# Optimization experiments

Hardware: AMD Instinct MI355X
Metric: run time of the kernel (lower is better)

Reference implementation:

```python
import jax, jax.numpy as jnp
import numpy as np


def setup_inputs() -> dict:
    key = jax.random.key(0)
    k1, k2 = jax.random.split(key)
    pred = jax.random.normal(k1, (1, 2048, 512), dtype=jnp.float32)
    cand = jax.random.normal(k2, (1, 65536, 512), dtype=jnp.float32)
    return {
        "predicted_transaction_company": pred,
        "future_transaction_companies_inc_current_data": cand,
    }


def reference(predicted_transaction_company, future_transaction_companies_inc_current_data):
    # torch.cdist with p=2 on [1,P,D] x [1,R,D] -> [1,P,R]; squeeze(0) -> [P,R]; global min.
    x = predicted_transaction_company[0]                       # [P, D]
    y = future_transaction_companies_inc_current_data[0]       # [R, D]
    sq = (
        jnp.sum(x * x, axis=-1)[:, None]
        + jnp.sum(y * y, axis=-1)[None, :]
        - 2.0 * jnp.einsum("pd,rd->pr", x, y)
    )                                                          # [P, R]
    distances = jnp.sqrt(jnp.maximum(sq, 0.0))
    return jnp.min(distances)
```

## Files before the change

### kernel.cpp

```cpp
#include <hip/hip_runtime.h>
#include <stdint.h>

#define P 2048
#define R 65536
#define DD 512
#define BT 128
#define BK 64

typedef __attribute__((ext_vector_type(8))) short short8;
typedef __attribute__((ext_vector_type(4))) float f32x4;

__device__ inline unsigned short f2bf(float f) {
  unsigned int u = __float_as_uint(f);
  u += 0x7fffu + ((u >> 16) & 1u);
  return (unsigned short)(u >> 16);
}

__device__ inline void gload_lds16(const void* g, void* l) {
  __builtin_amdgcn_global_load_lds(
      (const __attribute__((address_space(1))) unsigned int*)g,
      (__attribute__((address_space(3))) unsigned int*)l,
      16, 0, 0);
}

__global__ __launch_bounds__(256) void k_convert(
    const float* __restrict__ pred, const float* __restrict__ cand,
    unsigned short* __restrict__ Abf, unsigned short* __restrict__ Bbf,
    float* __restrict__ nx, float* __restrict__ ny,
    unsigned int* __restrict__ minp)
{
  if (blockIdx.x == 0 && threadIdx.x == 0) *minp = 0x7f800000u;
  int gw   = (blockIdx.x * 256 + threadIdx.x) >> 6;
  int lane = threadIdx.x & 63;
  if (gw >= P + R) return;
  const float* src; unsigned short* dst; float* np;
  if (gw < P) { src = pred + (size_t)gw * DD; dst = Abf + (size_t)gw * DD; np = nx + gw; }
  else { int r = gw - P; src = cand + (size_t)r * DD; dst = Bbf + (size_t)r * DD; np = ny + r; }
  const float4* s4 = ((const float4*)src) + lane * 2;
  float4 v0 = s4[0], v1 = s4[1];
  float ss = v0.x*v0.x + v0.y*v0.y + v0.z*v0.z + v0.w*v0.w
           + v1.x*v1.x + v1.y*v1.y + v1.z*v1.z + v1.w*v1.w;
  union { unsigned short h[8]; uint4 v; } pk;
  pk.h[0]=f2bf(v0.x); pk.h[1]=f2bf(v0.y); pk.h[2]=f2bf(v0.z); pk.h[3]=f2bf(v0.w);
  pk.h[4]=f2bf(v1.x); pk.h[5]=f2bf(v1.y); pk.h[6]=f2bf(v1.z); pk.h[7]=f2bf(v1.w);
  *(uint4*)(dst + (size_t)lane * 8) = pk.v;
  #pragma unroll
  for (int off = 32; off; off >>= 1) ss += __shfl_down(ss, off, 64);
  if (lane == 0) *np = ss;
}

__global__ __launch_bounds__(256) void k_gemm_min(
    const unsigned short* __restrict__ Abf, const unsigned short* __restrict__ Bbf,
    const float* __restrict__ nx, const float* __restrict__ ny,
    unsigned int* __restrict__ minp)
{
  __shared__ __align__(16) unsigned short As[BT * BK];
  __shared__ __align__(16) unsigned short Bs[BT * BK];
  __shared__ float wmin[4];

  const int tid  = threadIdx.x;
  const int wave = tid >> 6;
  const int lane = tid & 63;
  const int by = blockIdx.x & 15;
  const int bx = blockIdx.x >> 4;
  const int rowA0 = by * BT, rowB0 = bx * BT;
  const int wr = wave >> 1, wc = wave & 1;

  f32x4 zero = {0.f, 0.f, 0.f, 0.f};
  f32x4 acc[4][4];
  #pragma unroll
  for (int i = 0; i < 4; ++i)
    #pragma unroll
    for (int j = 0; j < 4; ++j) acc[i][j] = zero;

  const int rloc = lane >> 3;
  const int cswz = (lane & 7) ^ rloc;
  const unsigned short* gA[4]; const unsigned short* gB[4];
  unsigned short* lA[4]; unsigned short* lB[4];
  #pragma unroll
  for (int t = 0; t < 4; ++t) {
    const int rr = (wave * 4 + t) * 8 + rloc;
    gA[t] = Abf + (size_t)(rowA0 + rr) * DD + cswz * 8;
    gB[t] = Bbf + (size_t)(rowB0 + rr) * DD + cswz * 8;
    lA[t] = As + (wave * 4 + t) * 512;
    lB[t] = Bs + (wave * 4 + t) * 512;
  }

  const int m = lane & 15, quad = lane >> 4, mb = m & 7;
  const unsigned short* apB = As + (wr * 64 + m) * BK;
  const unsigned short* bpB = Bs + (wc * 64 + m) * BK;
  const int sw0 = ((quad    ) ^ mb) * 8;
  const int sw1 = ((quad + 4) ^ mb) * 8;

  for (int k0 = 0; k0 < DD; k0 += BK) {
    #pragma unroll
    for (int t = 0; t < 4; ++t) {
      gload_lds16(gA[t] + k0, lA[t]);
      gload_lds16(gB[t] + k0, lB[t]);
    }
    __syncthreads();

    short8 af[4], bfr[4];
    #pragma unroll
    for (int i = 0; i < 4; ++i) af[i]  = *(const short8*)(apB + i * 16 * BK + sw0);
    #pragma unroll
    for (int j = 0; j < 4; ++j) bfr[j] = *(const short8*)(bpB + j * 16 * BK + sw0);
    #pragma unroll
    for (int i = 0; i < 4; ++i)
      #pragma unroll
      for (int j = 0; j < 4; ++j)
        acc[i][j] = __builtin_amdgcn_mfma_f32_16x16x32_bf16(af[i], bfr[j], acc[i][j], 0, 0, 0);
    #pragma unroll
    for (int i = 0; i < 4; ++i) af[i]  = *(const short8*)(apB + i * 16 * BK + sw1);
    #pragma unroll
    for (int j = 0; j < 4; ++j) bfr[j] = *(const short8*)(bpB + j * 16 * BK + sw1);
    #pragma unroll
    for (int i = 0; i < 4; ++i)
      #pragma unroll
      for (int j = 0; j < 4; ++j)
        acc[i][j] = __builtin_amdgcn_mfma_f32_16x16x32_bf16(af[i], bfr[j], acc[i][j], 0, 0, 0);
    __syncthreads();
  }

  const int n16 = lane & 15;
  float lmin = 3.4e38f;
  #pragma unroll
  for (int i = 0; i < 4; ++i) {
    const int mbase = rowA0 + wr * 64 + i * 16 + quad * 4;
    float4 nxv = *(const float4*)(nx + mbase);
    #pragma unroll
    for (int j = 0; j < 4; ++j) {
      const int n = rowB0 + wc * 64 + j * 16 + n16;
      const float nyv = ny[n];
      f32x4 a = acc[i][j];
      lmin = fminf(lmin, nxv.x + nyv - 2.0f * a[0]);
      lmin = fminf(lmin, nxv.y + nyv - 2.0f * a[1]);
      lmin = fminf(lmin, nxv.z + nyv - 2.0f * a[2]);
      lmin = fminf(lmin, nxv.w + nyv - 2.0f * a[3]);
    }
  }
  #pragma unroll
  for (int off = 32; off; off >>= 1) lmin = fminf(lmin, __shfl_down(lmin, off, 64));
  if (lane == 0) wmin[wave] = lmin;
  __syncthreads();
  if (tid == 0) {
    float mn = fminf(fminf(wmin[0], wmin[1]), fminf(wmin[2], wmin[3]));
    atomicMin(minp, __float_as_uint(fmaxf(mn, 0.0f)));
  }
}

__global__ __launch_bounds__(64) void k_initmin(unsigned int* minp) {
  if (threadIdx.x == 0) *minp = 0x7f800000u;
}

__global__ __launch_bounds__(256) void k_brute(
    const float* __restrict__ pred, const float* __restrict__ cand,
    unsigned int* __restrict__ minp)
{
  __shared__ float yrow[DD];
  __shared__ float wm[4];
  const int c = blockIdx.x;
  for (int i = threadIdx.x; i < DD; i += 256) yrow[i] = cand[(size_t)c * DD + i];
  __syncthreads();
  float lmin = 3.4e38f;
  for (int p = threadIdx.x; p < P; p += 256) {
    const float* xp = pred + (size_t)p * DD;
    float s = 0.f;
    for (int k = 0; k < DD; ++k) { float d = xp[k] - yrow[k]; s = fmaf(d, d, s); }
    lmin = fminf(lmin, s);
  }
  #pragma unroll
  for (int off = 32; off; off >>= 1) lmin = fminf(lmin, __shfl_down(lmin, off, 64));
  if ((threadIdx.x & 63) == 0) wm[threadIdx.x >> 6] = lmin;
  __syncthreads();
  if (threadIdx.x == 0) {
    float mn = fminf(fminf(wm[0], wm[1]), fminf(wm[2], wm[3]));
    atomicMin(minp, __float_as_uint(fmaxf(mn, 0.0f)));
  }
}

__global__ __launch_bounds__(64) void k_finalize(const unsigned int* minp, float* out) {
  if (threadIdx.x == 0) out[0] = sqrtf(__uint_as_float(*minp));
}

extern "C" void kernel_launch(void* const* d_in, const int* in_sizes, int n_in,
                              void* d_out, int out_size, void* d_ws, size_t ws_size,
                              hipStream_t stream) {
  const float* pred = (const float*)d_in[0];
  const float* cand = (const float*)d_in[1];
  float* out = (float*)d_out;

  unsigned int* minp = (unsigned int*)d_ws;
  float* wsf = (float*)d_ws;
  float* nx = wsf + 16;
  float* ny = nx + P;
  unsigned short* Abf = (unsigned short*)(ny + R);
  unsigned short* Bbf = Abf + (size_t)P * DD;
  const size_t need = (size_t)(16 + P + R) * 4 + ((size_t)P * DD + (size_t)R * DD) * 2;

  if (ws_size >= need) {
    const int rows = P + R;
    k_convert<<<rows / 4, 256, 0, stream>>>(pred, cand, Abf, Bbf, nx, ny, minp);
    k_gemm_min<<<(P / BT) * (R / BT), 256, 0, stream>>>(Abf, Bbf, nx, ny, minp);
  } else {
    k_initmin<<<1, 64, 0, stream>>>(minp);
    k_brute<<<R, 256, 0, stream>>>(pred, cand, minp);
  }
  k_finalize<<<1, 64, 0, stream>>>(minp, out);
}
```

Baseline: 402.1 us.

## Use 256x256 double-buffered tiles with 8 waves and XCD-aware block remap

The GEMM tile grows from 128x128 with 4 waves to 256x256 with 8 waves. Each wave now computes 128x64, which raises arithmetic intensity per LDS byte. LDS is double-buffered so the next K-tile's global-to-LDS loads overlap the MFMAs, using explicit vmcnt waits and barriers, and s_setprio raises priority around the MFMA blocks. Blocks are remapped across XCDs for L2 locality of the A rows. The cost is higher register use (32 accumulators per lane), a 64KB LDS footprint, and reliance on hand-written waitcnt counts being correct.

```diff
diff --git a/kernel.cpp b/kernel.cpp
--- a/kernel.cpp
+++ b/kernel.cpp
@@ -4,8 +4,10 @@
 #define P 2048
 #define R 65536
 #define DD 512
-#define BT 128
+#define BM 256
+#define BN 256
 #define BK 64
+#define NT (DD / BK)
 
 typedef __attribute__((ext_vector_type(8))) short short8;
 typedef __attribute__((ext_vector_type(4))) float f32x4;
@@ -49,88 +51,119 @@
   if (lane == 0) *np = ss;
 }
 
-__global__ __launch_bounds__(256) void k_gemm_min(
+__global__ __launch_bounds__(512, 2) void k_gemm_min(
     const unsigned short* __restrict__ Abf, const unsigned short* __restrict__ Bbf,
     const float* __restrict__ nx, const float* __restrict__ ny,
     unsigned int* __restrict__ minp)
 {
-  __shared__ __align__(16) unsigned short As[BT * BK];
-  __shared__ __align__(16) unsigned short Bs[BT * BK];
-  __shared__ float wmin[4];
+  __shared__ __align__(16) unsigned short As[2][BM * BK];
+  __shared__ __align__(16) unsigned short Bs[2][BN * BK];
+  __shared__ float wmin[8];
 
   const int tid  = threadIdx.x;
   const int wave = tid >> 6;
   const int lane = tid & 63;
-  const int by = blockIdx.x & 15;
-  const int bx = blockIdx.x >> 4;
-  const int rowA0 = by * BT, rowB0 = bx * BT;
-  const int wr = wave >> 1, wc = wave & 1;
+
+  const int raw = blockIdx.x;
+  const int wg  = (raw & 7) * 256 + (raw >> 3);
+  const int by  = wg & 7;
+  const int bx  = wg >> 3;
+  const int rowA0 = by * BM, rowB0 = bx * BN;
+  const int wr = wave >> 2;
+  const int wc = wave & 3;
 
   f32x4 zero = {0.f, 0.f, 0.f, 0.f};
-  f32x4 acc[4][4];
-  #pragma unroll
-  for (int i = 0; i < 4; ++i)
+  f32x4 acc[8][4];
+  #pragma unroll
+  for (int i = 0; i < 8; ++i)
     #pragma unroll
     for (int j = 0; j < 4; ++j) acc[i][j] = zero;
 
   const int rloc = lane >> 3;
   const int cswz = (lane & 7) ^ rloc;
   const unsigned short* gA[4]; const unsigned short* gB[4];
-  unsigned short* lA[4]; unsigned short* lB[4];
+  int lOff[4];
   #pragma unroll
   for (int t = 0; t < 4; ++t) {
-    const int rr = (wave * 4 + t) * 8 + rloc;
+    const int ii = wave * 4 + t;
+    const int rr = ii * 8 + rloc;
     gA[t] = Abf + (size_t)(rowA0 + rr) * DD + cswz * 8;
     gB[t] = Bbf + (size_t)(rowB0 + rr) * DD + cswz * 8;
-    lA[t] = As + (wave * 4 + t) * 512;
-    lB[t] = Bs + (wave * 4 + t) * 512;
-  }
+    lOff[t] = ii * 512;
+  }
+
+#define STAGE(c, kt) do { const int _k0 = (kt) * BK;            \
+    _Pragma("unroll")                                           \
+    for (int _t = 0; _t < 4; ++_t) {                            \
+      gload_lds16(gA[_t] + _k0, &As[(c)][lOff[_t]]);            \
+      gload_lds16(gB[_t] + _k0, &Bs[(c)][lOff[_t]]);            \
+    } } while (0)
 
   const int m = lane & 15, quad = lane >> 4, mb = m & 7;
-  const unsigned short* apB = As + (wr * 64 + m) * BK;
-  const unsigned short* bpB = Bs + (wc * 64 + m) * BK;
-  const int sw0 = ((quad    ) ^ mb) * 8;
-  const int sw1 = ((quad + 4) ^ mb) * 8;
-
-  for (int k0 = 0; k0 < DD; k0 += BK) {
-    #pragma unroll
-    for (int t = 0; t < 4; ++t) {
-      gload_lds16(gA[t] + k0, lA[t]);
-      gload_lds16(gB[t] + k0, lB[t]);
-    }
-    __syncthreads();
-
-    short8 af[4], bfr[4];
-    #pragma unroll
-    for (int i = 0; i < 4; ++i) af[i]  = *(const short8*)(apB + i * 16 * BK + sw0);
-    #pragma unroll
-    for (int j = 0; j < 4; ++j) bfr[j] = *(const short8*)(bpB + j * 16 * BK + sw0);
-    #pragma unroll
-    for (int i = 0; i < 4; ++i)
+  const int aRow0 = (wr * 128 + m) * BK;
+  const int bRow0 = (wc * 64  + m) * BK;
+  const int swz0 = ((quad    ) ^ mb) * 8;
+  const int swz1 = ((quad + 4) ^ mb) * 8;
+
+  STAGE(0, 0);
+  STAGE(1, 1);
+  asm volatile("s_waitcnt vmcnt(8)" ::: "memory");
+  __builtin_amdgcn_s_barrier();
+
+  for (int kt = 0; kt < NT; ++kt) {
+    const int c = kt & 1;
+    const unsigned short* A0 = &As[c][0];
+    const unsigned short* B0 = &Bs[c][0];
+
+    short8 bfr[4][2];
+    #pragma unroll
+    for (int j = 0; j < 4; ++j) {
+      const unsigned short* bp = B0 + bRow0 + j * 16 * BK;
+      bfr[j][0] = *(const short8*)(bp + swz0);
+      bfr[j][1] = *(const short8*)(bp + swz1);
+    }
+    #pragma unroll
+    for (int mh = 0; mh < 2; ++mh) {
+      short8 af[4][2];
       #pragma unroll
-      for (int j = 0; j < 4; ++j)
-        acc[i][j] = __builtin_amdgcn_mfma_f32_16x16x32_bf16(af[i], bfr[j], acc[i][j], 0, 0, 0);
-    #pragma unroll
-    for (int i = 0; i < 4; ++i) af[i]  = *(const short8*)(apB + i * 16 * BK + sw1);
-    #pragma unroll
-    for (int j = 0; j < 4; ++j) bfr[j] = *(const short8*)(bpB + j * 16 * BK + sw1);
-    #pragma unroll
-    for (int i = 0; i < 4; ++i)
+      for (int i = 0; i < 4; ++i) {
+        const unsigned short* ap = A0 + aRow0 + (mh * 4 + i) * 16 * BK;
+        af[i][0] = *(const short8*)(ap + swz0);
+        af[i][1] = *(const short8*)(ap + swz1);
+      }
+      __builtin_amdgcn_s_setprio(1);
       #pragma unroll
-      for (int j = 0; j < 4; ++j)
-        acc[i][j] = __builtin_amdgcn_mfma_f32_16x16x32_bf16(af[i], bfr[j], acc[i][j], 0, 0, 0);
-    __syncthreads();
-  }
-
-  const int n16 = lane & 15;
+      for (int i = 0; i < 4; ++i)
+        #pragma unroll
+        for (int j = 0; j < 4; ++j) {
+          acc[mh*4+i][j] = __builtin_amdgcn_mfma_f32_16x16x32_bf16(af[i][0], bfr[j][0], acc[mh*4+i][j], 0, 0, 0);
+          acc[mh*4+i][j] = __builtin_amdgcn_mfma_f32_16x16x32_bf16(af[i][1], bfr[j][1], acc[mh*4+i][j], 0, 0, 0);
+        }
+      __builtin_amdgcn_s_setprio(0);
+      asm volatile("" ::: "memory");
+    }
+
+    if (kt < NT - 1) {
+      __builtin_amdgcn_s_barrier();
+      if (kt + 2 < NT) {
+        STAGE(c, kt + 2);
+        asm volatile("s_waitcnt vmcnt(8)" ::: "memory");
+      } else {
+        asm volatile("s_waitcnt vmcnt(0)" ::: "memory");
+      }
+      __builtin_amdgcn_s_barrier();
+    }
+  }
+#undef STAGE
+
   float lmin = 3.4e38f;
   #pragma unroll
-  for (int i = 0; i < 4; ++i) {
-    const int mbase = rowA0 + wr * 64 + i * 16 + quad * 4;
+  for (int i = 0; i < 8; ++i) {
+    const int mbase = rowA0 + wr * 128 + i * 16 + quad * 4;
     float4 nxv = *(const float4*)(nx + mbase);
     #pragma unroll
     for (int j = 0; j < 4; ++j) {
-      const int n = rowB0 + wc * 64 + j * 16 + n16;
+      const int n = rowB0 + wc * 64 + j * 16 + m;
       const float nyv = ny[n];
       f32x4 a = acc[i][j];
       lmin = fminf(lmin, nxv.x + nyv - 2.0f * a[0]);
@@ -144,7 +177,9 @@
   if (lane == 0) wmin[wave] = lmin;
   __syncthreads();
   if (tid == 0) {
-    float mn = fminf(fminf(wmin[0], wmin[1]), fminf(wmin[2], wmin[3]));
+    float mn = wmin[0];
+    #pragma unroll
+    for (int w = 1; w < 8; ++w) mn = fminf(mn, wmin[w]);
     atomicMin(minp, __float_as_uint(fmaxf(mn, 0.0f)));
   }
 }
@@ -201,7 +236,7 @@
   if (ws_size >= need) {
     const int rows = P + R;
     k_convert<<<rows / 4, 256, 0, stream>>>(pred, cand, Abf, Bbf, nx, ny, minp);
-    k_gemm_min<<<(P / BT) * (R / BT), 256, 0, stream>>>(Abf, Bbf, nx, ny, minp);
+    k_gemm_min<<<(P / BM) * (R / BN), 512, 0, stream>>>(Abf, Bbf, nx, ny, minp);
   } else {
     k_initmin<<<1, 64, 0, stream>>>(minp);
     k_brute<<<R, 256, 0, stream>>>(pred, cand, minp);
```

Measured after the change: 340.0 us. 1.18x faster.

## Double-buffer LDS tiles with BK=32 and XCD-aware block remapping in GEMM-min

Applied to the files above, without the earlier changes.

The GEMM-min kernel now uses two LDS stages with BK=32, so the next K tile is issued with global_load_lds before the current tile's MFMAs run. Explicit vmcnt waits and s_barrier replace __syncthreads. Blocks are remapped so consecutive workgroups on the same XCD share B tiles. The change also adds launch_bounds occupancy 4, s_setprio around MFMAs and a new LDS swizzle. The aim is to hide global-load latency and improve L2 locality, at the cost of more barriers per K step.

```diff
diff --git a/kernel.cpp b/kernel.cpp
--- a/kernel.cpp
+++ b/kernel.cpp
@@ -4,8 +4,10 @@
 #define P 2048
 #define R 65536
 #define DD 512
-#define BT 128
-#define BK 64
+#define BM 128
+#define BN 128
+#define BK 32
+#define NT (DD / BK)
 
 typedef __attribute__((ext_vector_type(8))) short short8;
 typedef __attribute__((ext_vector_type(4))) float f32x4;
@@ -49,22 +51,26 @@
   if (lane == 0) *np = ss;
 }
 
-__global__ __launch_bounds__(256) void k_gemm_min(
+__global__ __launch_bounds__(256, 4) void k_gemm_min(
     const unsigned short* __restrict__ Abf, const unsigned short* __restrict__ Bbf,
     const float* __restrict__ nx, const float* __restrict__ ny,
     unsigned int* __restrict__ minp)
 {
-  __shared__ __align__(16) unsigned short As[BT * BK];
-  __shared__ __align__(16) unsigned short Bs[BT * BK];
+  __shared__ __align__(16) unsigned short As[2][BM * BK];
+  __shared__ __align__(16) unsigned short Bs[2][BN * BK];
   __shared__ float wmin[4];
 
   const int tid  = threadIdx.x;
   const int wave = tid >> 6;
   const int lane = tid & 63;
-  const int by = blockIdx.x & 15;
-  const int bx = blockIdx.x >> 4;
-  const int rowA0 = by * BT, rowB0 = bx * BT;
-  const int wr = wave >> 1, wc = wave & 1;
+
+  const int raw = blockIdx.x;
+  const int wg  = (raw & 7) * 1024 + (raw >> 3);
+  const int by  = wg & 15;
+  const int bx  = wg >> 4;
+  const int rowA0 = by * BM, rowB0 = bx * BN;
+  const int wr = wave >> 1;
+  const int wc = wave & 1;
 
   f32x4 zero = {0.f, 0.f, 0.f, 0.f};
   f32x4 acc[4][4];
@@ -73,64 +79,66 @@
     #pragma unroll
     for (int j = 0; j < 4; ++j) acc[i][j] = zero;
 
-  const int rloc = lane >> 3;
-  const int cswz = (lane & 7) ^ rloc;
-  const unsigned short* gA[4]; const unsigned short* gB[4];
-  unsigned short* lA[4]; unsigned short* lB[4];
-  #pragma unroll
-  for (int t = 0; t < 4; ++t) {
-    const int rr = (wave * 4 + t) * 8 + rloc;
-    gA[t] = Abf + (size_t)(rowA0 + rr) * DD + cswz * 8;
-    gB[t] = Bbf + (size_t)(rowB0 + rr) * DD + cswz * 8;
-    lA[t] = As + (wave * 4 + t) * 512;
-    lB[t] = Bs + (wave * 4 + t) * 512;
-  }
-
-  const int m = lane & 15, quad = lane >> 4, mb = m & 7;
-  const unsigned short* apB = As + (wr * 64 + m) * BK;
-  const unsigned short* bpB = Bs + (wc * 64 + m) * BK;
-  const int sw0 = ((quad    ) ^ mb) * 8;
-  const int sw1 = ((quad + 4) ^ mb) * 8;
-
-  for (int k0 = 0; k0 < DD; k0 += BK) {
-    #pragma unroll
-    for (int t = 0; t < 4; ++t) {
-      gload_lds16(gA[t] + k0, lA[t]);
-      gload_lds16(gB[t] + k0, lB[t]);
+  const int rloc = lane >> 2;
+  const int csrc = (lane & 3) ^ ((lane >> 3) & 3);
+  const unsigned short* aS0 = Abf + (size_t)(rowA0 + wave * 32 + rloc) * DD + csrc * 8;
+  const unsigned short* aS1 = aS0 + 16 * DD;
+  const unsigned short* bS0 = Bbf + (size_t)(rowB0 + wave * 32 + rloc) * DD + csrc * 8;
+  const unsigned short* bS1 = bS0 + 16 * DD;
+  const int l0 = wave * 1024;
+  const int l1 = wave * 1024 + 512;
+
+#define STAGE(s, kk) do {                                   \
+    gload_lds16(aS0 + (kk), &As[s][l0]);                    \
+    gload_lds16(aS1 + (kk), &As[s][l1]);                    \
+    gload_lds16(bS0 + (kk), &Bs[s][l0]);                    \
+    gload_lds16(bS1 + (kk), &Bs[s][l1]);                    \
+  } while (0)
+
+  const int m = lane & 15, q = lane >> 4;
+  const int swc  = (q ^ ((m >> 1) & 3)) * 8;
+  const int aOff = (wr * 64 + m) * BK + swc;
+  const int bOff = (wc * 64 + m) * BK + swc;
+
+  STAGE(0, 0);
+
+  #pragma unroll 2
+  for (int T = 0; T < NT; ++T) {
+    const int s = T & 1;
+    if (T + 1 < NT) {
+      STAGE(s ^ 1, (T + 1) * BK);
+      asm volatile("s_waitcnt vmcnt(4)" ::: "memory");
+    } else {
+      asm volatile("s_waitcnt vmcnt(0)" ::: "memory");
     }
-    __syncthreads();
+    __builtin_amdgcn_s_barrier();
 
     short8 af[4], bfr[4];
     #pragma unroll
-    for (int i = 0; i < 4; ++i) af[i]  = *(const short8*)(apB + i * 16 * BK + sw0);
-    #pragma unroll
-    for (int j = 0; j < 4; ++j) bfr[j] = *(const short8*)(bpB + j * 16 * BK + sw0);
+    for (int i = 0; i < 4; ++i) af[i]  = *(const short8*)(&As[s][aOff + i * 16 * BK]);
+    #pragma unroll
+    for (int j = 0; j < 4; ++j) bfr[j] = *(const short8*)(&Bs[s][bOff + j * 16 * BK]);
+    asm volatile("s_waitcnt lgkmcnt(0)" ::: "memory");
+    __builtin_amdgcn_sched_barrier(0);
+    __builtin_amdgcn_s_setprio(1);
     #pragma unroll
     for (int i = 0; i < 4; ++i)
       #pragma unroll
       for (int j = 0; j < 4; ++j)
         acc[i][j] = __builtin_amdgcn_mfma_f32_16x16x32_bf16(af[i], bfr[j], acc[i][j], 0, 0, 0);
-    #pragma unroll
-    for (int i = 0; i < 4; ++i) af[i]  = *(const short8*)(apB + i * 16 * BK + sw1);
-    #pragma unroll
-    for (int j = 0; j < 4; ++j) bfr[j] = *(const short8*)(bpB + j * 16 * BK + sw1);
-    #pragma unroll
-    for (int i = 0; i < 4; ++i)
-      #pragma unroll
-      for (int j = 0; j < 4; ++j)
-        acc[i][j] = __builtin_amdgcn_mfma_f32_16x16x32_bf16(af[i], bfr[j], acc[i][j], 0, 0, 0);
-    __syncthreads();
-  }
-
-  const int n16 = lane & 15;
+    __builtin_amdgcn_s_setprio(0);
+    __builtin_amdgcn_s_barrier();
+  }
+#undef STAGE
+
   float lmin = 3.4e38f;
   #pragma unroll
   for (int i = 0; i < 4; ++i) {
-    const int mbase = rowA0 + wr * 64 + i * 16 + quad * 4;
+    const int mbase = rowA0 + wr * 64 + i * 16 + q * 4;
     float4 nxv = *(const float4*)(nx + mbase);
     #pragma unroll
     for (int j = 0; j < 4; ++j) {
-      const int n = rowB0 + wc * 64 + j * 16 + n16;
+      const int n = rowB0 + wc * 64 + j * 16 + m;
       const float nyv = ny[n];
       f32x4 a = acc[i][j];
       lmin = fminf(lmin, nxv.x + nyv - 2.0f * a[0]);
@@ -201,7 +209,7 @@
   if (ws_size >= need) {
     const int rows = P + R;
     k_convert<<<rows / 4, 256, 0, stream>>>(pred, cand, Abf, Bbf, nx, ny, minp);
-    k_gemm_min<<<(P / BT) * (R / BT), 256, 0, stream>>>(Abf, Bbf, nx, ny, minp);
+    k_gemm_min<<<(P / BM) * (R / BN), 256, 0, stream>>>(Abf, Bbf, nx, ny, minp);
   } else {
     k_initmin<<<1, 64, 0, stream>>>(minp);
     k_brute<<<R, 256, 0, stream>>>(pred, cand, minp);
```

Measured after the change: 381.0 us. 5.3% less time.
